# Optimization experiments

Hardware: AMD Instinct MI355X
Metric: run time of the kernel (lower is better)

Reference implementation:

```python
import jax, jax.numpy as jnp
import numpy as np

S, E, K = 100000, 30000, 1000
D, F = 64, 128
B = 16384
NNZ_S, NNZ_E, NNZ_K = 1600000, 480000, 32000
LAYERS = 3
MOMENTUM = 0.9
LEAK = 0.1


def setup_inputs() -> dict:
    key = jax.random.key(0)
    ks = jax.random.split(key, 24)
    inp = {}
    inp['student_id'] = jax.random.randint(ks[0], (B,), 0, S, dtype=jnp.int32)
    inp['exercise_id'] = jax.random.randint(ks[1], (B,), 0, E, dtype=jnp.int32)
    inp['q_mask'] = jnp.ones((B, K), jnp.float32)
    # embedding tables (xavier-ish scale)
    inp['stu_emb'] = jax.random.normal(ks[2], (S, D), jnp.float32) * 0.05
    inp['exer_emb'] = jax.random.normal(ks[3], (E, D), jnp.float32) * 0.05
    inp['know_emb'] = jax.random.normal(ks[4], (K, D), jnp.float32) * 0.05
    inp['impact_emb'] = jax.random.normal(ks[5], (E, D), jnp.float32) * 0.05
    # sparse adjacencies in COO form (rows, cols, vals); vals ~ normalized weights
    inp['s_rows'] = jax.random.randint(ks[6], (NNZ_S,), 0, S, dtype=jnp.int32)
    inp['s_cols'] = jax.random.randint(ks[7], (NNZ_S,), 0, S, dtype=jnp.int32)
    inp['s_vals'] = jax.random.uniform(ks[8], (NNZ_S,), jnp.float32) / 16.0
    inp['e_rows'] = jax.random.randint(ks[9], (NNZ_E,), 0, E, dtype=jnp.int32)
    inp['e_cols'] = jax.random.randint(ks[10], (NNZ_E,), 0, E, dtype=jnp.int32)
    inp['e_vals'] = jax.random.uniform(ks[11], (NNZ_E,), jnp.float32) / 16.0
    inp['k_rows'] = jax.random.randint(ks[12], (NNZ_K,), 0, K, dtype=jnp.int32)
    inp['k_cols'] = jax.random.randint(ks[13], (NNZ_K,), 0, K, dtype=jnp.int32)
    inp['k_vals'] = jax.random.uniform(ks[14], (NNZ_K,), jnp.float32) / 32.0
    # linear layers (stored as [in, out])
    inp['W_stu'] = jax.random.normal(ks[15], (D, F), jnp.float32) * 0.1
    inp['b_stu'] = jnp.zeros((F,), jnp.float32)
    inp['W_exer'] = jax.random.normal(ks[16], (D, F), jnp.float32) * 0.1
    inp['b_exer'] = jnp.zeros((F,), jnp.float32)
    inp['W_know'] = jax.random.normal(ks[17], (D, F), jnp.float32) * 0.1
    inp['b_know'] = jnp.zeros((F,), jnp.float32)
    inp['W_disc'] = jax.random.normal(ks[18], (D, 1), jnp.float32) * 0.1
    inp['b_disc'] = jnp.zeros((1,), jnp.float32)
    return inp


def spmm(rows, cols, vals, x, n):
    # sparse [n,n] @ dense [n,d] via gather + segment_sum
    return jax.ops.segment_sum(vals[:, None] * x[cols], rows, num_segments=n)


def convolution(emb, rows, cols, vals, n):
    # layers of SpMM with momentum residual; mean over all (layers+1) outputs
    acc = emb
    cur = emb
    for _ in range(LAYERS):
        cur = spmm(rows, cols, vals, cur, n) + MOMENTUM * cur
        acc = acc + cur
    return acc / (LAYERS + 1)


def reference(student_id, exercise_id, q_mask, stu_emb, exer_emb, know_emb,
              impact_emb, s_rows, s_cols, s_vals, e_rows, e_cols, e_vals,
              k_rows, k_cols, k_vals, W_stu, b_stu, W_exer, b_exer,
              W_know, b_know, W_disc, b_disc):
    stu_fwd = convolution(stu_emb, s_rows, s_cols, s_vals, S)    # [S, D]
    exer_fwd = convolution(exer_emb, e_rows, e_cols, e_vals, E)  # [E, D]
    know_fwd = convolution(know_emb, k_rows, k_cols, k_vals, K)  # [K, D]

    batch_student = stu_fwd[student_id]    # [B, D]
    batch_exercise = exer_fwd[exercise_id]  # [B, D]

    student_ts = jax.nn.leaky_relu(batch_student @ W_stu + b_stu, LEAK)   # [B, F]
    diff_ts = jax.nn.leaky_relu(batch_exercise @ W_exer + b_exer, LEAK)  # [B, F]
    knowledge_ts = jax.nn.leaky_relu(know_fwd @ W_know + b_know, LEAK)   # [K, F]
    disc_ts = jax.nn.sigmoid(batch_exercise @ W_disc + b_disc)          # [B, 1]

    student_ts = student_ts @ knowledge_ts.T  # [B, K]
    diff_ts = diff_ts @ knowledge_ts.T        # [B, K]
    knowledge_impact_ts = impact_emb[exercise_id]  # [B, D]
    return (student_ts, diff_ts, disc_ts, knowledge_ts, knowledge_impact_ts)
```

## Files before the change

### kernel.cpp

```cpp
#include <hip/hip_runtime.h>
#include <hip/hip_bf16.h>

#define S_N 100000
#define E_N 30000
#define K_N 1000
#define D_K 64
#define F_K 128
#define B_N 16384
#define NNZ_S 1600000
#define NNZ_E 480000
#define NNZ_K 32000
#define NNZ_TOT (NNZ_S + NNZ_E + NNZ_K)

#define NB_S 782
#define NB_E 235
#define NB_K 8
#define NB_TOT (NB_S + NB_E + NB_K)

#define CHUNK 4096
#define SB_S 391
#define SB_E 118
#define SB_K 8
#define SB_TOT (SB_S + SB_E + SB_K)

#define NCONV 8188
#define NGATH4 2111
#define GTOT4 540288
#define NIMP4 1024
#define FULLB 4094
#define LASTB 1056
#define NDENSE 4096
#define NKNOW 128
#define NDISC 4096

typedef __attribute__((ext_vector_type(8))) short sh8;
typedef __attribute__((ext_vector_type(4))) float f4;
typedef __attribute__((ext_vector_type(8))) unsigned short us8;

__device__ inline float b2f(ushort u) { return __uint_as_float((unsigned)u << 16); }
__device__ inline ushort f2b(float f) {
    unsigned u = __float_as_uint(f);
    return (ushort)((u + 0x7fffu + ((u >> 16) & 1u)) >> 16);
}

__global__ void pre_kernel(const float* __restrict__ stu_emb, const float* __restrict__ exer_emb,
                           const float* __restrict__ know_emb,
                           ushort* xb_s, ushort* xb_e, ushort* xb_k,
                           const int* __restrict__ sid, const int* __restrict__ eid,
                           float* bacc_s, float* bacc_e, float* kacc,
                           const int* __restrict__ sr, const int* __restrict__ er,
                           const int* __restrict__ kr, int* bcnt_tot,
                           const float* __restrict__ imp, float* out_imp) {
    int blk = blockIdx.x;
    int t = threadIdx.x;
    if (blk < NCONV) {
        const int NA = S_N * 64, NB = E_N * 64, NC = K_N * 64;
        int i = (blk * 256 + t) * 4;
        const float* src; ushort* dst;
        if (i < NA) { src = stu_emb; dst = xb_s; }
        else if (i < NA + NB) { i -= NA; src = exer_emb; dst = xb_e; }
        else if (i < NA + NB + NC) { i -= NA + NB; src = know_emb; dst = xb_k; }
        else return;
        float4 v = *(const float4*)&src[i];
        ushort4 o;
        o.x = f2b(v.x); o.y = f2b(v.y); o.z = f2b(v.z); o.w = f2b(v.w);
        *(ushort4*)&dst[i] = o;
    } else if (blk < NCONV + NGATH4) {
        int i4 = (blk - NCONV) * 256 + t;
        if (i4 >= GTOT4) return;
        int base = i4 * 4;
        const int BD = B_N * 64;
        if (base < BD) {
            int b = base >> 6, d0 = base & 63;
            *(float4*)&bacc_s[base] = *(const float4*)&stu_emb[(long)sid[b] * 64 + d0];
        } else if (base < 2 * BD) {
            int bb = base - BD; int b = bb >> 6, d0 = bb & 63;
            *(float4*)&bacc_e[bb] = *(const float4*)&exer_emb[(long)eid[b] * 64 + d0];
        } else {
            int bb = base - 2 * BD;
            *(float4*)&kacc[bb] = *(const float4*)&know_emb[bb];
        }
    } else if (blk < NCONV + NGATH4 + SB_TOT) {
        int lb = blk - NCONV - NGATH4;
        const int* rows; int boff, nnz, nb, lblk;
        if (lb < SB_S)            { lblk = lb;              rows = sr; boff = 0;           nnz = NNZ_S; nb = NB_S; }
        else if (lb < SB_S + SB_E){ lblk = lb - SB_S;       rows = er; boff = NB_S;        nnz = NNZ_E; nb = NB_E; }
        else                      { lblk = lb - SB_S - SB_E; rows = kr; boff = NB_S + NB_E; nnz = NNZ_K; nb = NB_K; }
        __shared__ int hist[NB_S];
        for (int i = t; i < nb; i += 256) hist[i] = 0;
        __syncthreads();
        int start = lblk * CHUNK, end = min(start + CHUNK, nnz);
        for (int i = start + t; i < end; i += 256) atomicAdd(&hist[rows[i] >> 7], 1);
        __syncthreads();
        for (int i = t; i < nb; i += 256) {
            int h = hist[i];
            if (h) atomicAdd(&bcnt_tot[boff + i], h);
        }
    } else {
        int i4 = (blk - NCONV - NGATH4 - SB_TOT) * 256 + t;
        if (i4 >= B_N * 16) return;
        int base = i4 * 4;
        int b = base >> 6, d0 = base & 63;
        *(float4*)&out_imp[base] = *(const float4*)&imp[(long)eid[b] * 64 + d0];
    }
}

__global__ void stage1_bin(const int* __restrict__ sr, const int* __restrict__ sc,
                           const float* __restrict__ sv,
                           const int* __restrict__ er, const int* __restrict__ ec,
                           const float* __restrict__ ev,
                           const int* __restrict__ kr, const int* __restrict__ kc,
                           const float* __restrict__ kv,
                           const int* __restrict__ bcnt_tot,
                           int* rsv, int2* stg_s, int2* stg_e, int2* stg_k) {
    int blk = blockIdx.x;
    const int* rows; const int* cols; const float* vals;
    int2* stg; int boff, nnz, nb, lblk;
    if (blk < SB_S) {
        lblk = blk; rows = sr; cols = sc; vals = sv; stg = stg_s;
        boff = 0; nnz = NNZ_S; nb = NB_S;
    } else if (blk < SB_S + SB_E) {
        lblk = blk - SB_S; rows = er; cols = ec; vals = ev; stg = stg_e;
        boff = NB_S; nnz = NNZ_E; nb = NB_E;
    } else {
        lblk = blk - SB_S - SB_E; rows = kr; cols = kc; vals = kv; stg = stg_k;
        boff = NB_S + NB_E; nnz = NNZ_K; nb = NB_K;
    }
    __shared__ int hist[NB_S];
    __shared__ int wbase[NB_S];
    __shared__ int base_l[NB_S];
    __shared__ int sc_s[256];
    int t = threadIdx.x;
    int lv[4]; int ls = 0;
    for (int j = 0; j < 4; j++) {
        int idx = t * 4 + j;
        lv[j] = (idx < nb) ? bcnt_tot[boff + idx] : 0;
        ls += lv[j];
    }
    sc_s[t] = ls; __syncthreads();
    for (int off = 1; off < 256; off <<= 1) {
        int x = (t >= off) ? sc_s[t - off] : 0;
        __syncthreads();
        sc_s[t] += x;
        __syncthreads();
    }
    int pre = sc_s[t] - ls;
    for (int j = 0; j < 4; j++) {
        int idx = t * 4 + j;
        if (idx < nb) { base_l[idx] = pre; pre += lv[j]; }
    }
    for (int i = t; i < nb; i += 256) hist[i] = 0;
    __syncthreads();
    int start = lblk * CHUNK, end = min(start + CHUNK, nnz);
    for (int i = start + t; i < end; i += 256) atomicAdd(&hist[rows[i] >> 7], 1);
    __syncthreads();
    for (int i = t; i < nb; i += 256) {
        int h = hist[i];
        int b0 = h ? atomicAdd(&rsv[boff + i], h) : 0;
        wbase[i] = base_l[i] + b0;
        hist[i] = 0;
    }
    __syncthreads();
    for (int i = start + t; i < end; i += 256) {
        int r = rows[i]; int b = r >> 7;
        int p = wbase[b] + atomicAdd(&hist[b], 1);
        stg[p] = make_int2(((r & 127) << 25) | cols[i], __float_as_int(vals[i]));
    }
}

__global__ void stage2_place(const int* __restrict__ bcnt_tot,
                             const int2* __restrict__ stg_s, int2* pr_s, int* rp_s,
                             const int2* __restrict__ stg_e, int2* pr_e, int* rp_e,
                             const int2* __restrict__ stg_k, int2* pr_k, int* rp_k) {
    int gb = blockIdx.x;
    int b = gb;
    const int2* stg; int2* pr; int* rp; int len, segbase, segnnz;
    if (b < NB_S) { stg = stg_s; pr = pr_s; rp = rp_s; len = S_N; segbase = 0; segnnz = NNZ_S; }
    else if (b < NB_S + NB_E) { b -= NB_S; stg = stg_e; pr = pr_e; rp = rp_e; len = E_N; segbase = NB_S; segnnz = NNZ_E; }
    else { b -= NB_S + NB_E; stg = stg_k; pr = pr_k; rp = rp_k; len = K_N; segbase = NB_S + NB_E; segnnz = NNZ_K; }
    int r0 = b << 7;
    int rows = min(128, len - r0);
    __shared__ int cnt[128];
    __shared__ int nx[128];
    __shared__ int red[256];
    int t = threadIdx.x;
    int s = 0;
    for (int i = t; i < b; i += 256) s += bcnt_tot[segbase + i];
    red[t] = s;
    if (t < 128) cnt[t] = 0;
    __syncthreads();
    for (int off = 128; off > 0; off >>= 1) {
        if (t < off) red[t] += red[t + off];
        __syncthreads();
    }
    int j0 = red[0];
    int j1 = j0 + bcnt_tot[segbase + b];
    if (b == 0 && t == 0) rp[len] = segnnz;
    for (int j = j0 + t; j < j1; j += 256)
        atomicAdd(&cnt[((unsigned)stg[j].x) >> 25], 1);
    __syncthreads();
    int my = (t < 128) ? cnt[t] : 0;
    for (int off = 1; off < 128; off <<= 1) {
        int y = (t < 128 && t >= off) ? cnt[t - off] : 0;
        __syncthreads();
        if (t < 128) cnt[t] += y;
        __syncthreads();
    }
    if (t < 128) {
        int ex = j0 + cnt[t] - my;
        nx[t] = ex;
        if (t < rows) rp[r0 + t] = ex;
    }
    __syncthreads();
    for (int j = j0 + t; j < j1; j += 256) {
        int2 e = stg[j];
        int r_rel = ((unsigned)e.x) >> 25;
        int col = e.x & 0x01FFFFFF;
        int p = atomicAdd(&nx[r_rel], 1);
        pr[p] = make_int2(col, e.y);
    }
}

__device__ __forceinline__ void spmm_row_compute(
        const int* __restrict__ rp, const int2* __restrict__ pr,
        const ushort* __restrict__ x, int r, int l, float* a) {
    const us8* __restrict__ X8 = (const us8*)x;
    int j0 = rp[r], j1 = rp[r + 1];
    us8 self = X8[r * 8 + l];
    #pragma unroll
    for (int k = 0; k < 8; k++) a[k] = 0.9f * b2f(self[k]);
    int j = j0;
    for (; j + 8 <= j1; j += 8) {
        int2 q[8]; us8 v[8];
        #pragma unroll
        for (int u = 0; u < 8; u++) q[u] = pr[j + u];
        #pragma unroll
        for (int u = 0; u < 8; u++) v[u] = X8[q[u].x * 8 + l];
        #pragma unroll
        for (int u = 0; u < 8; u++) {
            float w = __int_as_float(q[u].y);
            #pragma unroll
            for (int k = 0; k < 8; k++) a[k] = fmaf(w, b2f(v[u][k]), a[k]);
        }
    }
    if (j + 4 <= j1) {
        int2 q[4]; us8 v[4];
        #pragma unroll
        for (int u = 0; u < 4; u++) q[u] = pr[j + u];
        #pragma unroll
        for (int u = 0; u < 4; u++) v[u] = X8[q[u].x * 8 + l];
        #pragma unroll
        for (int u = 0; u < 4; u++) {
            float w = __int_as_float(q[u].y);
            #pragma unroll
            for (int k = 0; k < 8; k++) a[k] = fmaf(w, b2f(v[u][k]), a[k]);
        }
        j += 4;
    }
    if (j < j1) {
        int last = j1 - 1;
        int2 q[4]; us8 v[4]; float w[4];
        #pragma unroll
        for (int u = 0; u < 4; u++) q[u] = pr[min(j + u, last)];
        #pragma unroll
        for (int u = 0; u < 4; u++) v[u] = X8[q[u].x * 8 + l];
        #pragma unroll
        for (int u = 0; u < 4; u++) w[u] = (j + u <= last) ? __int_as_float(q[u].y) : 0.f;
        #pragma unroll
        for (int u = 0; u < 4; u++) {
            #pragma unroll
            for (int k = 0; k < 8; k++) a[k] = fmaf(w[u], b2f(v[u][k]), a[k]);
        }
    }
}

__device__ __forceinline__ void spmm_store(ushort* y, int row, int l, const float* a) {
    us8 o;
    #pragma unroll
    for (int k = 0; k < 8; k++) o[k] = f2b(a[k]);
    *(us8*)&y[row * 64 + l * 8] = o;
}

__device__ __forceinline__ void spmm_full_body(
        int blk0, int t,
        const int* __restrict__ rp_s, const int2* __restrict__ pr_s,
        const ushort* __restrict__ xs, ushort* ys,
        const int* __restrict__ rp_e, const int2* __restrict__ pr_e,
        const ushort* __restrict__ xe, ushort* ye,
        const int* __restrict__ rp_k, const int2* __restrict__ pr_k,
        const ushort* __restrict__ xk, ushort* yk) {
    int w = (blk0 * 256 + t) >> 3;
    int l = t & 7;
    const int* rp; const int2* pr; const ushort* x; ushort* y; int r;
    if (w < S_N) { rp = rp_s; pr = pr_s; x = xs; y = ys; r = w; }
    else if (w < S_N + E_N) { rp = rp_e; pr = pr_e; x = xe; y = ye; r = w - S_N; }
    else if (w < S_N + E_N + K_N) { rp = rp_k; pr = pr_k; x = xk; y = yk; r = w - S_N - E_N; }
    else return;
    float a[8];
    spmm_row_compute(rp, pr, x, r, l, a);
    spmm_store(y, r, l, a);
}

__device__ __forceinline__ void gather_accb_body4(
        int i4, const int* __restrict__ sid, const int* __restrict__ eid,
        const ushort* __restrict__ src_s, const ushort* __restrict__ src_e,
        const ushort* __restrict__ src_k,
        float* bacc_s, float* bacc_e, float* kacc) {
    if (i4 >= GTOT4) return;
    int base = i4 * 4;
    const int BD = B_N * 64;
    const ushort* src; float* acc; long soff; int aoff;
    if (base < BD) {
        int b = base >> 6, d0 = base & 63;
        src = src_s; acc = bacc_s; soff = (long)sid[b] * 64 + d0; aoff = base;
    } else if (base < 2 * BD) {
        int bb = base - BD; int b = bb >> 6, d0 = bb & 63;
        src = src_e; acc = bacc_e; soff = (long)eid[b] * 64 + d0; aoff = bb;
    } else {
        int bb = base - 2 * BD;
        src = src_k; acc = kacc; soff = bb; aoff = bb;
    }
    ushort4 v = *(const ushort4*)&src[soff];
    float4 a = *(const float4*)&acc[aoff];
    a.x += b2f(v.x); a.y += b2f(v.y); a.z += b2f(v.z); a.w += b2f(v.w);
    *(float4*)&acc[aoff] = a;
}

__global__ void spmm_l1(const int* __restrict__ rp_s, const int2* __restrict__ pr_s,
                        const ushort* __restrict__ xs, ushort* ys,
                        const int* __restrict__ rp_e, const int2* __restrict__ pr_e,
                        const ushort* __restrict__ xe, ushort* ye,
                        const int* __restrict__ rp_k, const int2* __restrict__ pr_k,
                        const ushort* __restrict__ xk, ushort* yk) {
    spmm_full_body(blockIdx.x, threadIdx.x, rp_s, pr_s, xs, ys,
                   rp_e, pr_e, xe, ye, rp_k, pr_k, xk, yk);
}

__global__ void spmm_l2_fused(const int* __restrict__ rp_s, const int2* __restrict__ pr_s,
                              const ushort* __restrict__ xs, ushort* ys,
                              const int* __restrict__ rp_e, const int2* __restrict__ pr_e,
                              const ushort* __restrict__ xe, ushort* ye,
                              const int* __restrict__ rp_k, const int2* __restrict__ pr_k,
                              const ushort* __restrict__ xk, ushort* yk,
                              const int* __restrict__ sid, const int* __restrict__ eid,
                              float* bacc_s, float* bacc_e, float* kacc) {
    int blk = blockIdx.x;
    if (blk < FULLB) {
        spmm_full_body(blk, threadIdx.x, rp_s, pr_s, xs, ys,
                       rp_e, pr_e, xe, ye, rp_k, pr_k, xk, yk);
    } else {
        int i4 = (blk - FULLB) * 256 + threadIdx.x;
        gather_accb_body4(i4, sid, eid, xs, xe, xk, bacc_s, bacc_e, kacc);
    }
}

__global__ void spmm_l3_fused(const int* __restrict__ sid, const int* __restrict__ eid,
                              const int* __restrict__ rp_s, const int2* __restrict__ pr_s,
                              const ushort* __restrict__ xs, ushort* c3s,
                              const int* __restrict__ rp_e, const int2* __restrict__ pr_e,
                              const ushort* __restrict__ xe, ushort* c3e,
                              const int* __restrict__ rp_k, const int2* __restrict__ pr_k,
                              const ushort* __restrict__ xk, ushort* yk,
                              float* bacc_s, float* bacc_e, float* kacc) {
    int blk = blockIdx.x;
    int t = threadIdx.x;
    if (blk < LASTB) {
        int w = (blk * 256 + t) >> 3;
        int l = t & 7;
        const int* rp; const int2* pr; const ushort* x; ushort* y; int r; int orow;
        if (w < B_N) { rp = rp_s; pr = pr_s; x = xs; y = c3s; r = sid[w]; orow = w; }
        else if (w < 2 * B_N) {
            int b = w - B_N;
            rp = rp_e; pr = pr_e; x = xe; y = c3e; r = eid[b]; orow = b;
        } else if (w < 2 * B_N + K_N) {
            r = w - 2 * B_N;
            rp = rp_k; pr = pr_k; x = xk; y = yk; orow = r;
        } else return;
        float a[8];
        spmm_row_compute(rp, pr, x, r, l, a);
        spmm_store(y, orow, l, a);
    } else {
        int i4 = (blk - LASTB) * 256 + t;
        gather_accb_body4(i4, sid, eid, xs, xe, xk, bacc_s, bacc_e, kacc);
    }
}

__global__ void post_kernel(const float* __restrict__ bacc_s, const ushort* __restrict__ c3_s,
                            const float* __restrict__ bacc_e, const ushort* __restrict__ c3_e,
                            const float* __restrict__ W_stu, const float* __restrict__ b_stu,
                            const float* __restrict__ W_exer, const float* __restrict__ b_exer,
                            __hip_bfloat16* st_b, __hip_bfloat16* df_b,
                            const float* __restrict__ kacc, const ushort* __restrict__ cur3_k,
                            const float* __restrict__ W_know, const float* __restrict__ b_know,
                            float* out_kn_f32, __hip_bfloat16* kn_b,
                            const float* __restrict__ W_disc, const float* __restrict__ b_disc,
                            float* out_disc) {
    int blk = blockIdx.x;
    int t = threadIdx.x;
    if (blk < NDENSE) {
        int which = blk >> 11;
        int local = blk & 2047;
        const float* bacc = which ? bacc_e : bacc_s;
        const ushort* c3 = which ? c3_e : c3_s;
        const float* W = which ? W_exer : W_stu;
        const float* bias = which ? b_exer : b_stu;
        __hip_bfloat16* out = which ? df_b : st_b;
        int r0 = local * 8;
        __shared__ float X[8][64];
        for (int i = t; i < 512; i += 256) {
            int lr = i >> 6, d = i & 63; int b = r0 + lr;
            X[lr][d] = 0.25f * (bacc[(long)b * 64 + d] + b2f(c3[(long)b * 64 + d]));
        }
        __syncthreads();
        int lr = t >> 7, f = t & 127;
        float acc[4];
        #pragma unroll
        for (int rr = 0; rr < 4; rr++) acc[rr] = bias[f];
        for (int d = 0; d < 64; d++) {
            float wv = W[d * 128 + f];
            #pragma unroll
            for (int rr = 0; rr < 4; rr++) acc[rr] += X[rr * 2 + lr][d] * wv;
        }
        #pragma unroll
        for (int rr = 0; rr < 4; rr++) {
            float a = acc[rr];
            a = a > 0.f ? a : 0.1f * a;
            out[(long)(r0 + rr * 2 + lr) * 128 + f] = __float2bfloat16(a);
        }
    } else if (blk < NDENSE + NKNOW) {
        int r0 = (blk - NDENSE) * 8;
        __shared__ float X[8][64];
        for (int i = t; i < 512; i += 256) {
            int lr = i >> 6, d = i & 63; int r = r0 + lr;
            X[lr][d] = (r < K_N) ? 0.25f * (kacc[r * 64 + d] + b2f(cur3_k[r * 64 + d])) : 0.f;
        }
        __syncthreads();
        int lr = t >> 7, f = t & 127;
        float acc[4];
        #pragma unroll
        for (int rr = 0; rr < 4; rr++) acc[rr] = b_know[f];
        for (int d = 0; d < 64; d++) {
            float wv = W_know[d * 128 + f];
            #pragma unroll
            for (int rr = 0; rr < 4; rr++) acc[rr] += X[rr * 2 + lr][d] * wv;
        }
        #pragma unroll
        for (int rr = 0; rr < 4; rr++) {
            int r = r0 + rr * 2 + lr;
            float a = acc[rr];
            a = a > 0.f ? a : 0.1f * a;
            if (r < K_N) {
                out_kn_f32[(long)r * 128 + f] = a;
                kn_b[(long)r * 128 + f] = __float2bfloat16(a);
            } else {
                kn_b[(long)r * 128 + f] = __float2bfloat16(0.f);
            }
        }
    } else {
        int w = ((blk - NDENSE - NKNOW) * 256 + t) >> 6;
        int d = t & 63;
        if (w >= B_N) return;
        float x = 0.25f * (bacc_e[(long)w * 64 + d] + b2f(c3_e[(long)w * 64 + d])) * W_disc[d];
        for (int off = 32; off > 0; off >>= 1) x += __shfl_down(x, off, 64);
        if (d == 0) {
            float z = x + b_disc[0];
            out_disc[w] = 1.f / (1.f + expf(-z));
        }
    }
}

__global__ void big_mm(const __hip_bfloat16* __restrict__ st, const __hip_bfloat16* __restrict__ df,
                       const __hip_bfloat16* __restrict__ kn,
                       float* __restrict__ out0, float* __restrict__ out1) {
    const ushort* X = (const ushort*)(blockIdx.z ? df : st);
    const ushort* Kn = (const ushort*)kn;
    float* out = blockIdx.z ? out1 : out0;
    int wv = threadIdx.x >> 6;
    int lane = threadIdx.x & 63;
    int m_blk = blockIdx.y * 64 + (wv >> 1) * 32;
    int n_blk = blockIdx.x * 256 + (wv & 1) * 128;
    int q = lane >> 4, l16 = lane & 15;
    f4 acc0[8], acc1[8];
    #pragma unroll
    for (int nt = 0; nt < 8; nt++) { acc0[nt] = {0.f, 0.f, 0.f, 0.f}; acc1[nt] = acc0[nt]; }
    for (int s = 0; s < 4; s++) {
        int kofs = s * 32 + q * 8;
        sh8 a0 = *(const sh8*)&X[(long)(m_blk + l16) * 128 + kofs];
        sh8 a1 = *(const sh8*)&X[(long)(m_blk + 16 + l16) * 128 + kofs];
        #pragma unroll
        for (int nt = 0; nt < 8; nt++) {
            sh8 bb = *(const sh8*)&Kn[(long)(n_blk + nt * 16 + l16) * 128 + kofs];
            acc0[nt] = __builtin_amdgcn_mfma_f32_16x16x32_bf16(a0, bb, acc0[nt], 0, 0, 0);
            acc1[nt] = __builtin_amdgcn_mfma_f32_16x16x32_bf16(a1, bb, acc1[nt], 0, 0, 0);
        }
    }
    #pragma unroll
    for (int nt = 0; nt < 8; nt++) {
        int col = n_blk + nt * 16 + l16;
        if (col >= K_N) continue;
        #pragma unroll
        for (int r = 0; r < 4; r++) {
            out[(long)(m_blk + q * 4 + r) * K_N + col] = acc0[nt][r];
            out[(long)(m_blk + 16 + q * 4 + r) * K_N + col] = acc1[nt][r];
        }
    }
}

extern "C" void kernel_launch(void* const* d_in, const int* in_sizes, int n_in,
                              void* d_out, int out_size, void* d_ws, size_t ws_size,
                              hipStream_t stream) {
    const int* sid = (const int*)d_in[0];
    const int* eid = (const int*)d_in[1];
    const float* stu_emb = (const float*)d_in[3];
    const float* exer_emb = (const float*)d_in[4];
    const float* know_emb = (const float*)d_in[5];
    const float* impact_emb = (const float*)d_in[6];
    const int* s_rows = (const int*)d_in[7];
    const int* s_cols = (const int*)d_in[8];
    const float* s_vals = (const float*)d_in[9];
    const int* e_rows = (const int*)d_in[10];
    const int* e_cols = (const int*)d_in[11];
    const float* e_vals = (const float*)d_in[12];
    const int* k_rows = (const int*)d_in[13];
    const int* k_cols = (const int*)d_in[14];
    const float* k_vals = (const float*)d_in[15];
    const float* W_stu = (const float*)d_in[16];
    const float* b_stu = (const float*)d_in[17];
    const float* W_exer = (const float*)d_in[18];
    const float* b_exer = (const float*)d_in[19];
    const float* W_know = (const float*)d_in[20];
    const float* b_know = (const float*)d_in[21];
    const float* W_disc = (const float*)d_in[22];
    const float* b_disc = (const float*)d_in[23];

    float* out = (float*)d_out;
    float* out_st = out;
    float* out_df = out + 16384000;
    float* out_disc = out + 32768000;
    float* out_kn = out + 32784384;
    float* out_imp = out + 32912384;

    char* p = (char*)d_ws;
    auto alloc = [&](size_t bytes) -> char* {
        char* r = p;
        p += (bytes + 255) & ~(size_t)255;
        return r;
    };
    ushort* xb_s = (ushort*)alloc((size_t)S_N * 64 * 2);
    ushort* xb_e = (ushort*)alloc((size_t)E_N * 64 * 2);
    ushort* xb_k = (ushort*)alloc((size_t)K_N * 64 * 2);
    ushort* bufA_s = (ushort*)alloc((size_t)S_N * 64 * 2);
    ushort* bufB_s = (ushort*)alloc((size_t)S_N * 64 * 2);
    ushort* bufA_e = (ushort*)alloc((size_t)E_N * 64 * 2);
    ushort* bufB_e = (ushort*)alloc((size_t)E_N * 64 * 2);
    ushort* bufA_k = (ushort*)alloc((size_t)K_N * 64 * 2);
    ushort* bufB_k = (ushort*)alloc((size_t)K_N * 64 * 2);
    ushort* c3s = (ushort*)alloc((size_t)B_N * 64 * 2);
    ushort* c3e = (ushort*)alloc((size_t)B_N * 64 * 2);
    float* bacc_s = (float*)alloc((size_t)B_N * 64 * 4);
    float* bacc_e = (float*)alloc((size_t)B_N * 64 * 4);
    float* kacc = (float*)alloc((size_t)K_N * 64 * 4);
    __hip_bfloat16* st_b = (__hip_bfloat16*)alloc((size_t)B_N * 128 * 2);
    __hip_bfloat16* df_b = (__hip_bfloat16*)alloc((size_t)B_N * 128 * 2);
    __hip_bfloat16* kn_b = (__hip_bfloat16*)alloc((size_t)1024 * 128 * 2);
    int* bcnt_tot = (int*)alloc((size_t)2 * NB_TOT * 4);
    int* rsv = bcnt_tot + NB_TOT;
    int* rp_s = (int*)alloc((size_t)(S_N + 1) * 4);
    int* rp_e = (int*)alloc((size_t)(E_N + 1) * 4);
    int* rp_k = (int*)alloc((size_t)(K_N + 1) * 4);
    int2* stg_s = (int2*)alloc((size_t)NNZ_S * 8);
    int2* stg_e = (int2*)alloc((size_t)NNZ_E * 8);
    int2* stg_k = (int2*)alloc((size_t)NNZ_K * 8);
    int2* pr_s = (int2*)alloc((size_t)NNZ_S * 8);
    int2* pr_e = (int2*)alloc((size_t)NNZ_E * 8);
    int2* pr_k = (int2*)alloc((size_t)NNZ_K * 8);

    hipMemsetAsync(bcnt_tot, 0, (size_t)2 * NB_TOT * 4, stream);
    pre_kernel<<<NCONV + NGATH4 + SB_TOT + NIMP4, 256, 0, stream>>>(
        stu_emb, exer_emb, know_emb, xb_s, xb_e, xb_k,
        sid, eid, bacc_s, bacc_e, kacc,
        s_rows, e_rows, k_rows, bcnt_tot, impact_emb, out_imp);
    stage1_bin<<<SB_TOT, 256, 0, stream>>>(
        s_rows, s_cols, s_vals, e_rows, e_cols, e_vals, k_rows, k_cols, k_vals,
        bcnt_tot, rsv, stg_s, stg_e, stg_k);
    stage2_place<<<NB_TOT, 256, 0, stream>>>(bcnt_tot,
                                             stg_s, pr_s, rp_s,
                                             stg_e, pr_e, rp_e,
                                             stg_k, pr_k, rp_k);
    spmm_l1<<<FULLB, 256, 0, stream>>>(rp_s, pr_s, xb_s, bufA_s,
                                       rp_e, pr_e, xb_e, bufA_e,
                                       rp_k, pr_k, xb_k, bufA_k);
    spmm_l2_fused<<<FULLB + NGATH4, 256, 0, stream>>>(
        rp_s, pr_s, bufA_s, bufB_s,
        rp_e, pr_e, bufA_e, bufB_e,
        rp_k, pr_k, bufA_k, bufB_k,
        sid, eid, bacc_s, bacc_e, kacc);
    spmm_l3_fused<<<LASTB + NGATH4, 256, 0, stream>>>(
        sid, eid,
        rp_s, pr_s, bufB_s, c3s,
        rp_e, pr_e, bufB_e, c3e,
        rp_k, pr_k, bufB_k, bufA_k,
        bacc_s, bacc_e, kacc);
    post_kernel<<<NDENSE + NKNOW + NDISC, 256, 0, stream>>>(
        bacc_s, c3s, bacc_e, c3e, W_stu, b_stu, W_exer, b_exer, st_b, df_b,
        kacc, bufA_k, W_know, b_know, out_kn, kn_b,
        W_disc, b_disc, out_disc);
    big_mm<<<dim3(4, B_N / 64, 2), 256, 0, stream>>>(st_b, df_b, kn_b, out_st, out_df);
}
```

Baseline: 544.1 us.

## Fuse CSR placement with first SpMM layer per 128-row bin

The CSR placement kernel (stage2) now computes the first propagation layer for its own 128-row bin right after scattering entries, using the per-row end offsets kept in shared memory. The separate spmm_l1 launch is removed. This saves one kernel launch and lets layer 1 read the freshly written pr entries while they may still sit in cache. In exchange each block does more serial work, with only 32 row-groups per 256 threads, so parallelism and load balance in layer 1 may suffer.

```diff
diff --git a/kernel.cpp b/kernel.cpp
--- a/kernel.cpp
+++ b/kernel.cpp
@@ -168,16 +168,85 @@
     }
 }
 
-__global__ void stage2_place(const int* __restrict__ bcnt_tot,
-                             const int2* __restrict__ stg_s, int2* pr_s, int* rp_s,
-                             const int2* __restrict__ stg_e, int2* pr_e, int* rp_e,
-                             const int2* __restrict__ stg_k, int2* pr_k, int* rp_k) {
+__device__ __forceinline__ void spmm_row_range(
+        const int2* __restrict__ pr, int j0r, int j1r,
+        const ushort* __restrict__ x, int r, int l, float* a) {
+    const us8* __restrict__ X8 = (const us8*)x;
+    us8 self = X8[r * 8 + l];
+    #pragma unroll
+    for (int k = 0; k < 8; k++) a[k] = 0.9f * b2f(self[k]);
+    int j = j0r;
+    for (; j + 8 <= j1r; j += 8) {
+        int2 q[8]; us8 v[8];
+        #pragma unroll
+        for (int u = 0; u < 8; u++) q[u] = pr[j + u];
+        #pragma unroll
+        for (int u = 0; u < 8; u++) v[u] = X8[q[u].x * 8 + l];
+        #pragma unroll
+        for (int u = 0; u < 8; u++) {
+            float w = __int_as_float(q[u].y);
+            #pragma unroll
+            for (int k = 0; k < 8; k++) a[k] = fmaf(w, b2f(v[u][k]), a[k]);
+        }
+    }
+    if (j + 4 <= j1r) {
+        int2 q[4]; us8 v[4];
+        #pragma unroll
+        for (int u = 0; u < 4; u++) q[u] = pr[j + u];
+        #pragma unroll
+        for (int u = 0; u < 4; u++) v[u] = X8[q[u].x * 8 + l];
+        #pragma unroll
+        for (int u = 0; u < 4; u++) {
+            float w = __int_as_float(q[u].y);
+            #pragma unroll
+            for (int k = 0; k < 8; k++) a[k] = fmaf(w, b2f(v[u][k]), a[k]);
+        }
+        j += 4;
+    }
+    if (j < j1r) {
+        int last = j1r - 1;
+        int2 q[4]; us8 v[4]; float w[4];
+        #pragma unroll
+        for (int u = 0; u < 4; u++) q[u] = pr[min(j + u, last)];
+        #pragma unroll
+        for (int u = 0; u < 4; u++) v[u] = X8[q[u].x * 8 + l];
+        #pragma unroll
+        for (int u = 0; u < 4; u++) w[u] = (j + u <= last) ? __int_as_float(q[u].y) : 0.f;
+        #pragma unroll
+        for (int u = 0; u < 4; u++) {
+            #pragma unroll
+            for (int k = 0; k < 8; k++) a[k] = fmaf(w[u], b2f(v[u][k]), a[k]);
+        }
+    }
+}
+
+__device__ __forceinline__ void spmm_row_compute(
+        const int* __restrict__ rp, const int2* __restrict__ pr,
+        const ushort* __restrict__ x, int r, int l, float* a) {
+    spmm_row_range(pr, rp[r], rp[r + 1], x, r, l, a);
+}
+
+__device__ __forceinline__ void spmm_store(ushort* y, int row, int l, const float* a) {
+    us8 o;
+    #pragma unroll
+    for (int k = 0; k < 8; k++) o[k] = f2b(a[k]);
+    *(us8*)&y[row * 64 + l * 8] = o;
+}
+
+__global__ void stage2_spmm(const int* __restrict__ bcnt_tot,
+                            const int2* __restrict__ stg_s, int2* pr_s, int* rp_s,
+                            const ushort* __restrict__ xs, ushort* ys,
+                            const int2* __restrict__ stg_e, int2* pr_e, int* rp_e,
+                            const ushort* __restrict__ xe, ushort* ye,
+                            const int2* __restrict__ stg_k, int2* pr_k, int* rp_k,
+                            const ushort* __restrict__ xk, ushort* yk) {
     int gb = blockIdx.x;
     int b = gb;
-    const int2* stg; int2* pr; int* rp; int len, segbase, segnnz;
-    if (b < NB_S) { stg = stg_s; pr = pr_s; rp = rp_s; len = S_N; segbase = 0; segnnz = NNZ_S; }
-    else if (b < NB_S + NB_E) { b -= NB_S; stg = stg_e; pr = pr_e; rp = rp_e; len = E_N; segbase = NB_S; segnnz = NNZ_E; }
-    else { b -= NB_S + NB_E; stg = stg_k; pr = pr_k; rp = rp_k; len = K_N; segbase = NB_S + NB_E; segnnz = NNZ_K; }
+    const int2* stg; int2* pr; int* rp; const ushort* x; ushort* y;
+    int len, segbase, segnnz;
+    if (b < NB_S) { stg = stg_s; pr = pr_s; rp = rp_s; x = xs; y = ys; len = S_N; segbase = 0; segnnz = NNZ_S; }
+    else if (b < NB_S + NB_E) { b -= NB_S; stg = stg_e; pr = pr_e; rp = rp_e; x = xe; y = ye; len = E_N; segbase = NB_S; segnnz = NNZ_E; }
+    else { b -= NB_S + NB_E; stg = stg_k; pr = pr_k; rp = rp_k; x = xk; y = yk; len = K_N; segbase = NB_S + NB_E; segnnz = NNZ_K; }
     int r0 = b << 7;
     int rows = min(128, len - r0);
     __shared__ int cnt[128];
@@ -201,9 +270,9 @@
     __syncthreads();
     int my = (t < 128) ? cnt[t] : 0;
     for (int off = 1; off < 128; off <<= 1) {
-        int y = (t < 128 && t >= off) ? cnt[t - off] : 0;
-        __syncthreads();
-        if (t < 128) cnt[t] += y;
+        int y2 = (t < 128 && t >= off) ? cnt[t - off] : 0;
+        __syncthreads();
+        if (t < 128) cnt[t] += y2;
         __syncthreads();
     }
     if (t < 128) {
@@ -219,66 +288,16 @@
         int p = atomicAdd(&nx[r_rel], 1);
         pr[p] = make_int2(col, e.y);
     }
-}
-
-__device__ __forceinline__ void spmm_row_compute(
-        const int* __restrict__ rp, const int2* __restrict__ pr,
-        const ushort* __restrict__ x, int r, int l, float* a) {
-    const us8* __restrict__ X8 = (const us8*)x;
-    int j0 = rp[r], j1 = rp[r + 1];
-    us8 self = X8[r * 8 + l];
-    #pragma unroll
-    for (int k = 0; k < 8; k++) a[k] = 0.9f * b2f(self[k]);
-    int j = j0;
-    for (; j + 8 <= j1; j += 8) {
-        int2 q[8]; us8 v[8];
-        #pragma unroll
-        for (int u = 0; u < 8; u++) q[u] = pr[j + u];
-        #pragma unroll
-        for (int u = 0; u < 8; u++) v[u] = X8[q[u].x * 8 + l];
-        #pragma unroll
-        for (int u = 0; u < 8; u++) {
-            float w = __int_as_float(q[u].y);
-            #pragma unroll
-            for (int k = 0; k < 8; k++) a[k] = fmaf(w, b2f(v[u][k]), a[k]);
-        }
-    }
-    if (j + 4 <= j1) {
-        int2 q[4]; us8 v[4];
-        #pragma unroll
-        for (int u = 0; u < 4; u++) q[u] = pr[j + u];
-        #pragma unroll
-        for (int u = 0; u < 4; u++) v[u] = X8[q[u].x * 8 + l];
-        #pragma unroll
-        for (int u = 0; u < 4; u++) {
-            float w = __int_as_float(q[u].y);
-            #pragma unroll
-            for (int k = 0; k < 8; k++) a[k] = fmaf(w, b2f(v[u][k]), a[k]);
-        }
-        j += 4;
-    }
-    if (j < j1) {
-        int last = j1 - 1;
-        int2 q[4]; us8 v[4]; float w[4];
-        #pragma unroll
-        for (int u = 0; u < 4; u++) q[u] = pr[min(j + u, last)];
-        #pragma unroll
-        for (int u = 0; u < 4; u++) v[u] = X8[q[u].x * 8 + l];
-        #pragma unroll
-        for (int u = 0; u < 4; u++) w[u] = (j + u <= last) ? __int_as_float(q[u].y) : 0.f;
-        #pragma unroll
-        for (int u = 0; u < 4; u++) {
-            #pragma unroll
-            for (int k = 0; k < 8; k++) a[k] = fmaf(w[u], b2f(v[u][k]), a[k]);
-        }
-    }
-}
-
-__device__ __forceinline__ void spmm_store(ushort* y, int row, int l, const float* a) {
-    us8 o;
-    #pragma unroll
-    for (int k = 0; k < 8; k++) o[k] = f2b(a[k]);
-    *(us8*)&y[row * 64 + l * 8] = o;
+    __syncthreads();
+    int l = t & 7;
+    for (int rl = t >> 3; rl < rows; rl += 32) {
+        int j0r = (rl == 0) ? j0 : nx[rl - 1];
+        int j1r = nx[rl];
+        int r = r0 + rl;
+        float a[8];
+        spmm_row_range(pr, j0r, j1r, x, r, l, a);
+        spmm_store(y, r, l, a);
+    }
 }
 
 __device__ __forceinline__ void spmm_full_body(
@@ -324,16 +343,6 @@
     float4 a = *(const float4*)&acc[aoff];
     a.x += b2f(v.x); a.y += b2f(v.y); a.z += b2f(v.z); a.w += b2f(v.w);
     *(float4*)&acc[aoff] = a;
-}
-
-__global__ void spmm_l1(const int* __restrict__ rp_s, const int2* __restrict__ pr_s,
-                        const ushort* __restrict__ xs, ushort* ys,
-                        const int* __restrict__ rp_e, const int2* __restrict__ pr_e,
-                        const ushort* __restrict__ xe, ushort* ye,
-                        const int* __restrict__ rp_k, const int2* __restrict__ pr_k,
-                        const ushort* __restrict__ xk, ushort* yk) {
-    spmm_full_body(blockIdx.x, threadIdx.x, rp_s, pr_s, xs, ys,
-                   rp_e, pr_e, xe, ye, rp_k, pr_k, xk, yk);
 }
 
 __global__ void spmm_l2_fused(const int* __restrict__ rp_s, const int2* __restrict__ pr_s,
@@ -583,13 +592,10 @@
     stage1_bin<<<SB_TOT, 256, 0, stream>>>(
         s_rows, s_cols, s_vals, e_rows, e_cols, e_vals, k_rows, k_cols, k_vals,
         bcnt_tot, rsv, stg_s, stg_e, stg_k);
-    stage2_place<<<NB_TOT, 256, 0, stream>>>(bcnt_tot,
-                                             stg_s, pr_s, rp_s,
-                                             stg_e, pr_e, rp_e,
-                                             stg_k, pr_k, rp_k);
-    spmm_l1<<<FULLB, 256, 0, stream>>>(rp_s, pr_s, xb_s, bufA_s,
-                                       rp_e, pr_e, xb_e, bufA_e,
-                                       rp_k, pr_k, xb_k, bufA_k);
+    stage2_spmm<<<NB_TOT, 256, 0, stream>>>(bcnt_tot,
+                                            stg_s, pr_s, rp_s, xb_s, bufA_s,
+                                            stg_e, pr_e, rp_e, xb_e, bufA_e,
+                                            stg_k, pr_k, rp_k, xb_k, bufA_k);
     spmm_l2_fused<<<FULLB + NGATH4, 256, 0, stream>>>(
         rp_s, pr_s, bufA_s, bufB_s,
         rp_e, pr_e, bufA_e, bufB_e,
```

After: 555.4 us. +2.1%, slower.
